# Kernel optimization log

Measured on AMD Instinct MI355X. Metric: run time of the kernel, lower is better.

The kernel has to match this reference:

```python
import jax, jax.numpy as jnp
import numpy as np

HEAD_COUNT = 16


def setup_inputs() -> dict:
    key = jax.random.key(0)
    ks = jax.random.split(key, 9)
    B, T, C = 2, 2048, 1024
    s = 1.0 / np.sqrt(C)
    x = jax.random.normal(ks[0], (B, T, C), dtype=jnp.float32)
    Wq = jax.random.normal(ks[1], (C, C), dtype=jnp.float32) * s
    bq = jnp.zeros((C,), dtype=jnp.float32)
    Wk = jax.random.normal(ks[2], (C, C), dtype=jnp.float32) * s
    bk = jnp.zeros((C,), dtype=jnp.float32)
    Wv = jax.random.normal(ks[3], (C, C), dtype=jnp.float32) * s
    bv = jnp.zeros((C,), dtype=jnp.float32)
    Wp = jax.random.normal(ks[4], (C, C), dtype=jnp.float32) * s
    bp = jnp.zeros((C,), dtype=jnp.float32)
    return {"x": x, "Wq": Wq, "bq": bq, "Wk": Wk, "bk": bk,
            "Wv": Wv, "bv": bv, "Wp": Wp, "bp": bp}


def reference(x, Wq, bq, Wk, bk, Wv, bv, Wp, bp):
    B, T, C = x.shape
    H = HEAD_COUNT
    D = C // H
    # Linear projections (torch Linear: y = x W^T + b) -> [B, H, T, D]
    def proj(W, b):
        y = jnp.einsum('btc,dc->btd', x, W) + b
        return y.reshape(B, T, H, D).transpose(0, 2, 1, 3)
    q = proj(Wq, bq)
    k = proj(Wk, bk)
    v = proj(Wv, bv)
    # Scaled dot-product attention with causal mask
    att = jnp.einsum('bhqd,bhkd->bhqk', q, k) * (1.0 / np.sqrt(D))
    causal = jnp.tril(jnp.ones((T, T), dtype=bool))  # [T, T]
    att = jnp.where(causal[None, None], att, -jnp.inf)
    att = jax.nn.softmax(att, axis=-1)
    # attention dropout p=0.0 (eval equivalent): identity
    y = jnp.einsum('bhqk,bhkd->bhqd', att, v)
    y = y.transpose(0, 2, 1, 3).reshape(B, T, C)
    # output projection + residual dropout p=0.0
    out = jnp.einsum('btc,dc->btd', y, Wp) + bp
    return out
```

## Files before the change

kernel.cpp:

```cpp
#include <hip/hip_runtime.h>
#include <math.h>

#define BATCH 2
#define SEQ   2048
#define CDIM  1024
#define NH    16
#define HD    64

typedef _Float16 half8 __attribute__((ext_vector_type(8)));
typedef _Float16 half4 __attribute__((ext_vector_type(4)));
typedef float    f32x4 __attribute__((ext_vector_type(4)));

#define LDH 72

typedef const __attribute__((address_space(1))) void* gas_ptr;
typedef __attribute__((address_space(3))) void* las_ptr;

__device__ __forceinline__ void gld16(const _Float16* g, _Float16* l) {
    __builtin_amdgcn_global_load_lds((gas_ptr)g, (las_ptr)l, 16, 0, 0);
}

__device__ inline half8 cvt8(float4 a, float4 b) {
    half8 h;
    h[0] = (_Float16)a.x; h[1] = (_Float16)a.y; h[2] = (_Float16)a.z; h[3] = (_Float16)a.w;
    h[4] = (_Float16)b.x; h[5] = (_Float16)b.y; h[6] = (_Float16)b.z; h[7] = (_Float16)b.w;
    return h;
}

__global__ __launch_bounds__(256) void cvt_all(
    const float* __restrict__ x,
    const float* __restrict__ Wq, const float* __restrict__ Wk,
    const float* __restrict__ Wv, const float* __restrict__ Wp,
    _Float16* __restrict__ x16, _Float16* __restrict__ w16,
    _Float16* __restrict__ wp16)
{
    int c = blockIdx.x * 256 + threadIdx.x;
    const float* src;
    _Float16* dst;
    if (c < 524288) {
        src = x + (size_t)c * 8;
        dst = x16 + (size_t)c * 8;
    } else {
        int r = c - 524288;
        int w = r >> 17;
        size_t off = (size_t)(r & 131071) * 8;
        if (w == 0)      { src = Wq + off; dst = w16 + off; }
        else if (w == 1) { src = Wk + off; dst = w16 + (1u << 20) + off; }
        else if (w == 2) { src = Wv + off; dst = w16 + (2u << 20) + off; }
        else             { src = Wp + off; dst = wp16 + off; }
    }
    float4 a = *(const float4*)src;
    float4 b = *(const float4*)(src + 4);
    *(half8*)dst = cvt8(a, b);
}

__global__ __launch_bounds__(256) void qkv_gemm(
    const _Float16* __restrict__ x16, const _Float16* __restrict__ w16,
    const float* __restrict__ bq, const float* __restrict__ bk,
    const float* __restrict__ bv,
    _Float16* __restrict__ q, _Float16* __restrict__ k, _Float16* __restrict__ v)
{
    __shared__ _Float16 Ash[128 * 64];
    __shared__ _Float16 Bsh[128 * 64];

    const int tid  = threadIdx.x;
    const int lane = tid & 63;
    const int wave = tid >> 6;
    const int wm = wave >> 1;
    const int wn = wave & 1;
    const int lg = lane >> 4;
    const int lr = lane & 15;

    const int m0 = blockIdx.x * 128;
    const int nG = blockIdx.y * 128;
    const int w  = nG >> 10;

    const int srow = lane >> 3;
    const int scol = (lane & 7) * 8;

    f32x4 acc[4][4];
#pragma unroll
    for (int m = 0; m < 4; ++m)
#pragma unroll
        for (int n = 0; n < 4; ++n) acc[m][n] = (f32x4)0.0f;

    for (int kt = 0; kt < CDIM; kt += 64) {
        __syncthreads();
#pragma unroll
        for (int i = 0; i < 4; ++i) {
            int chunk = wave * 4 + i;
            int row = chunk * 8 + srow;
            gld16(x16 + (size_t)(m0 + row) * CDIM + kt + scol, Ash + chunk * 512);
            gld16(w16 + (size_t)(nG + row) * CDIM + kt + scol, Bsh + chunk * 512);
        }
        __syncthreads();
#pragma unroll
        for (int kk = 0; kk < 2; ++kk) {
            half8 af[4], bf[4];
#pragma unroll
            for (int m = 0; m < 4; ++m)
                af[m] = *(half8*)&Ash[(wm * 64 + m * 16 + lr) * 64 + kk * 32 + lg * 8];
#pragma unroll
            for (int n = 0; n < 4; ++n)
                bf[n] = *(half8*)&Bsh[(wn * 64 + n * 16 + lr) * 64 + kk * 32 + lg * 8];
#pragma unroll
            for (int m = 0; m < 4; ++m)
#pragma unroll
                for (int n = 0; n < 4; ++n)
                    acc[m][n] = __builtin_amdgcn_mfma_f32_16x16x32_f16(af[m], bf[n], acc[m][n], 0, 0, 0);
        }
    }

    const float* bias = (w == 0) ? bq : (w == 1) ? bk : bv;
    _Float16* dst     = (w == 0) ? q  : (w == 1) ? k  : v;
    const float qs    = (w == 0) ? 0.125f : 1.0f;
    const int n0 = nG & 1023;

#pragma unroll
    for (int n = 0; n < 4; ++n) {
        int col = n0 + wn * 64 + n * 16 + lr;
        float bv_ = bias[col];
        int h = col >> 6, d = col & 63;
#pragma unroll
        for (int m = 0; m < 4; ++m) {
#pragma unroll
            for (int i = 0; i < 4; ++i) {
                int mr = m0 + wm * 64 + m * 16 + lg * 4 + i;
                int bb = mr >> 11;
                int t  = mr & (SEQ - 1);
                dst[((size_t)(bb * NH + h) * SEQ + t) * HD + d] =
                    (_Float16)((acc[m][n][i] + bv_) * qs);
            }
        }
    }
}

__global__ __launch_bounds__(256) void proj_gemm(
    const _Float16* __restrict__ y16, const _Float16* __restrict__ wp16,
    const float* __restrict__ bp, float* __restrict__ out)
{
    __shared__ _Float16 Ash[128 * 64];
    __shared__ _Float16 Bsh[64 * 64];

    const int tid  = threadIdx.x;
    const int lane = tid & 63;
    const int wave = tid >> 6;
    const int wm = wave >> 1;
    const int wn = wave & 1;
    const int lg = lane >> 4;
    const int lr = lane & 15;

    const int m0 = blockIdx.x * 128;
    const int n0 = blockIdx.y * 64;

    const int srow = lane >> 3;
    const int scol = (lane & 7) * 8;

    f32x4 acc[4][2];
#pragma unroll
    for (int m = 0; m < 4; ++m)
#pragma unroll
        for (int n = 0; n < 2; ++n) acc[m][n] = (f32x4)0.0f;

    for (int kt = 0; kt < CDIM; kt += 64) {
        __syncthreads();
#pragma unroll
        for (int i = 0; i < 4; ++i) {
            int chunk = wave * 4 + i;
            int row = chunk * 8 + srow;
            gld16(y16 + (size_t)(m0 + row) * CDIM + kt + scol, Ash + chunk * 512);
        }
#pragma unroll
        for (int i = 0; i < 2; ++i) {
            int chunk = wave * 2 + i;
            int row = chunk * 8 + srow;
            gld16(wp16 + (size_t)(n0 + row) * CDIM + kt + scol, Bsh + chunk * 512);
        }
        __syncthreads();
#pragma unroll
        for (int kk = 0; kk < 2; ++kk) {
            half8 af[4], bf[2];
#pragma unroll
            for (int m = 0; m < 4; ++m)
                af[m] = *(half8*)&Ash[(wm * 64 + m * 16 + lr) * 64 + kk * 32 + lg * 8];
#pragma unroll
            for (int n = 0; n < 2; ++n)
                bf[n] = *(half8*)&Bsh[(wn * 32 + n * 16 + lr) * 64 + kk * 32 + lg * 8];
#pragma unroll
            for (int m = 0; m < 4; ++m)
#pragma unroll
                for (int n = 0; n < 2; ++n)
                    acc[m][n] = __builtin_amdgcn_mfma_f32_16x16x32_f16(af[m], bf[n], acc[m][n], 0, 0, 0);
        }
    }

#pragma unroll
    for (int n = 0; n < 2; ++n) {
        int col = n0 + wn * 32 + n * 16 + lr;
        float bv_ = bp[col];
#pragma unroll
        for (int m = 0; m < 4; ++m) {
#pragma unroll
            for (int i = 0; i < 4; ++i) {
                int mr = m0 + wm * 64 + m * 16 + lg * 4 + i;
                out[(size_t)mr * CDIM + col] = acc[m][n][i] + bv_;
            }
        }
    }
}

__global__ __launch_bounds__(256) void attn_kernel(
    const _Float16* __restrict__ q, const _Float16* __restrict__ k,
    const _Float16* __restrict__ v, _Float16* __restrict__ y)
{
    __shared__ _Float16 Kt[64 * 64];
    __shared__ _Float16 Vt[64 * LDH];
    __shared__ _Float16 Pt[4][32 * LDH];

    const int tid  = threadIdx.x;
    const int lane = tid & 63;
    const int wave = tid >> 6;
    const int lg = lane >> 4;
    const int lr = lane & 15;

    const int qt  = gridDim.x - 1 - blockIdx.x;
    const int bh  = blockIdx.y;
    const int q0  = qt * 128;
    const int q0w = q0 + wave * 32;

    const _Float16* qb = q + (size_t)bh * SEQ * HD;
    const _Float16* kb = k + (size_t)bh * SEQ * HD;
    const _Float16* vb = v + (size_t)bh * SEQ * HD;

    half8 qfr[2][2];
#pragma unroll
    for (int f = 0; f < 2; ++f)
#pragma unroll
        for (int kk = 0; kk < 2; ++kk)
            qfr[f][kk] = *(const half8*)(qb + (size_t)(q0w + f * 16 + lr) * HD + kk * 32 + lg * 8);

    f32x4 ot[4][2];
#pragma unroll
    for (int df = 0; df < 4; ++df)
#pragma unroll
        for (int qf = 0; qf < 2; ++qf) ot[df][qf] = (f32x4)0.0f;
    float m_i[2] = {-INFINITY, -INFINITY};
    float l_i[2] = {0.0f, 0.0f};

    const int vd0  = (tid & 15) * 4;
    const int vkv0 = (tid >> 4) * 4;

    const int ntiles = 2 * qt + 2;
    for (int kt = 0; kt < ntiles; ++kt) {
        const int k0 = kt * 64;
        __syncthreads();
#pragma unroll
        for (int i = 0; i < 2; ++i) {
            int chunk = wave * 2 + i;
            int row = chunk * 8 + (lane >> 3);
            gld16(kb + (size_t)(k0 + row) * HD + (lane & 7) * 8, Kt + chunk * 512);
        }
        {
            half4 r0 = *(const half4*)(vb + (size_t)(k0 + vkv0 + 0) * HD + vd0);
            half4 r1 = *(const half4*)(vb + (size_t)(k0 + vkv0 + 1) * HD + vd0);
            half4 r2 = *(const half4*)(vb + (size_t)(k0 + vkv0 + 2) * HD + vd0);
            half4 r3 = *(const half4*)(vb + (size_t)(k0 + vkv0 + 3) * HD + vd0);
            half4 c;
#pragma unroll
            for (int j = 0; j < 4; ++j) {
                c[0] = r0[j]; c[1] = r1[j]; c[2] = r2[j]; c[3] = r3[j];
                *(half4*)&Vt[(vd0 + j) * LDH + vkv0] = c;
            }
        }
        __syncthreads();

        f32x4 st[4][2];
#pragma unroll
        for (int mf = 0; mf < 4; ++mf)
#pragma unroll
            for (int qf = 0; qf < 2; ++qf) st[mf][qf] = (f32x4)0.0f;
#pragma unroll
        for (int kk = 0; kk < 2; ++kk) {
#pragma unroll
            for (int mf = 0; mf < 4; ++mf) {
                half8 ak = *(half8*)&Kt[(mf * 16 + lr) * 64 + kk * 32 + lg * 8];
#pragma unroll
                for (int qf = 0; qf < 2; ++qf)
                    st[mf][qf] = __builtin_amdgcn_mfma_f32_16x16x32_f16(ak, qfr[qf][kk], st[mf][qf], 0, 0, 0);
            }
        }

        if (k0 + 63 > q0w) {
#pragma unroll
            for (int mf = 0; mf < 4; ++mf)
#pragma unroll
                for (int qf = 0; qf < 2; ++qf)
#pragma unroll
                    for (int i = 0; i < 4; ++i) {
                        int kv = k0 + mf * 16 + lg * 4 + i;
                        int qq = q0w + qf * 16 + lr;
                        if (kv > qq) st[mf][qf][i] = -INFINITY;
                    }
        }

#pragma unroll
        for (int qf = 0; qf < 2; ++qf) {
            float mx = -INFINITY;
#pragma unroll
            for (int mf = 0; mf < 4; ++mf)
#pragma unroll
                for (int i = 0; i < 4; ++i) mx = fmaxf(mx, st[mf][qf][i]);
            mx = fmaxf(mx, __shfl_xor(mx, 16));
            mx = fmaxf(mx, __shfl_xor(mx, 32));
            float nm = fmaxf(m_i[qf], mx);
            float sc = __expf(m_i[qf] - nm);
            m_i[qf] = nm;
            float rs = 0.0f;
#pragma unroll
            for (int mf = 0; mf < 4; ++mf) {
                half4 pk;
#pragma unroll
                for (int i = 0; i < 4; ++i) {
                    float p = __expf(st[mf][qf][i] - nm);
                    rs += p;
                    pk[i] = (_Float16)p;
                }
                *(half4*)&Pt[wave][(qf * 16 + lr) * LDH + mf * 16 + lg * 4] = pk;
            }
            rs += __shfl_xor(rs, 16);
            rs += __shfl_xor(rs, 32);
            l_i[qf] = l_i[qf] * sc + rs;
#pragma unroll
            for (int df = 0; df < 4; ++df)
#pragma unroll
                for (int i = 0; i < 4; ++i) ot[df][qf][i] *= sc;
        }

#pragma unroll
        for (int kk = 0; kk < 2; ++kk) {
            half8 bp_[2];
#pragma unroll
            for (int qf = 0; qf < 2; ++qf)
                bp_[qf] = *(half8*)&Pt[wave][(qf * 16 + lr) * LDH + kk * 32 + lg * 8];
#pragma unroll
            for (int df = 0; df < 4; ++df) {
                half8 av = *(half8*)&Vt[(df * 16 + lr) * LDH + kk * 32 + lg * 8];
#pragma unroll
                for (int qf = 0; qf < 2; ++qf)
                    ot[df][qf] = __builtin_amdgcn_mfma_f32_16x16x32_f16(av, bp_[qf], ot[df][qf], 0, 0, 0);
            }
        }
    }

    const int bb = bh >> 4;
    const int h  = bh & 15;
#pragma unroll
    for (int qf = 0; qf < 2; ++qf) {
        float inv = 1.0f / l_i[qf];
        int t = q0w + qf * 16 + lr;
        _Float16* dst = y + ((size_t)(bb * SEQ + t)) * CDIM + h * HD;
#pragma unroll
        for (int df = 0; df < 4; ++df) {
            half4 o4;
#pragma unroll
            for (int i = 0; i < 4; ++i) o4[i] = (_Float16)(ot[df][qf][i] * inv);
            *(half4*)(dst + df * 16 + lg * 4) = o4;
        }
    }
}

extern "C" void kernel_launch(void* const* d_in, const int* in_sizes, int n_in,
                              void* d_out, int out_size, void* d_ws, size_t ws_size,
                              hipStream_t stream) {
    const float* x  = (const float*)d_in[0];
    const float* Wq = (const float*)d_in[1];
    const float* bq = (const float*)d_in[2];
    const float* Wk = (const float*)d_in[3];
    const float* bk = (const float*)d_in[4];
    const float* Wv = (const float*)d_in[5];
    const float* bv = (const float*)d_in[6];
    const float* Wp = (const float*)d_in[7];
    const float* bp = (const float*)d_in[8];
    float* out = (float*)d_out;

    const size_t S = (size_t)BATCH * SEQ * CDIM;
    _Float16* ws = (_Float16*)d_ws;
    _Float16* x16  = ws;
    _Float16* w16  = x16 + S;
    _Float16* wp16 = w16 + 3 * CDIM * CDIM;
    _Float16* qbuf = wp16 + CDIM * CDIM;
    _Float16* kbuf = qbuf + S;
    _Float16* vbuf = kbuf + S;
    _Float16* ybuf = vbuf + S;

    cvt_all<<<4096, 256, 0, stream>>>(x, Wq, Wk, Wv, Wp, x16, w16, wp16);

    qkv_gemm<<<dim3(4096 / 128, 3072 / 128), 256, 0, stream>>>(
        x16, w16, bq, bk, bv, qbuf, kbuf, vbuf);

    attn_kernel<<<dim3(SEQ / 128, BATCH * NH), 256, 0, stream>>>(
        qbuf, kbuf, vbuf, ybuf);

    proj_gemm<<<dim3(4096 / 128, 1024 / 64), 256, 0, stream>>>(
        ybuf, wp16, bp, out);
}
```

Baseline: 243.5 us.

## Split attention block into eight waves of 16 queries with swizzled K tile

The attention kernel now launches 512 threads per block, so each wave owns 16 query rows instead of 32. This halves per-wave register state and gives more waves to hide latency. Waves whose query rows lie entirely before the current key tile now skip that tile's QK^T, softmax and PV work, which trims causal-mask waste. The K tile in LDS uses an XOR swizzle to reduce bank conflicts, and V staging is split across more threads. In exchange, each K/V tile loaded into LDS is reused by fewer query rows per wave, MFMA operand reuse drops, and the higher thread count may limit occupancy.

Result: faster. 225.6 us (-7.3%).

```diff
diff --git a/kernel.cpp b/kernel.cpp
--- a/kernel.cpp
+++ b/kernel.cpp
@@ -9,6 +9,7 @@
 
 typedef _Float16 half8 __attribute__((ext_vector_type(8)));
 typedef _Float16 half4 __attribute__((ext_vector_type(4)));
+typedef _Float16 half2v __attribute__((ext_vector_type(2)));
 typedef float    f32x4 __attribute__((ext_vector_type(4)));
 
 #define LDH 72
@@ -209,13 +210,13 @@
     }
 }
 
-__global__ __launch_bounds__(256) void attn_kernel(
+__global__ __launch_bounds__(512) void attn_kernel(
     const _Float16* __restrict__ q, const _Float16* __restrict__ k,
     const _Float16* __restrict__ v, _Float16* __restrict__ y)
 {
     __shared__ _Float16 Kt[64 * 64];
     __shared__ _Float16 Vt[64 * LDH];
-    __shared__ _Float16 Pt[4][32 * LDH];
+    __shared__ _Float16 Pt[8][16 * LDH];
 
     const int tid  = threadIdx.x;
     const int lane = tid & 63;
@@ -226,146 +227,121 @@
     const int qt  = gridDim.x - 1 - blockIdx.x;
     const int bh  = blockIdx.y;
     const int q0  = qt * 128;
-    const int q0w = q0 + wave * 32;
+    const int q0w = q0 + wave * 16;
 
     const _Float16* qb = q + (size_t)bh * SEQ * HD;
     const _Float16* kb = k + (size_t)bh * SEQ * HD;
     const _Float16* vb = v + (size_t)bh * SEQ * HD;
 
-    half8 qfr[2][2];
-#pragma unroll
-    for (int f = 0; f < 2; ++f)
-#pragma unroll
-        for (int kk = 0; kk < 2; ++kk)
-            qfr[f][kk] = *(const half8*)(qb + (size_t)(q0w + f * 16 + lr) * HD + kk * 32 + lg * 8);
-
-    f32x4 ot[4][2];
-#pragma unroll
-    for (int df = 0; df < 4; ++df)
-#pragma unroll
-        for (int qf = 0; qf < 2; ++qf) ot[df][qf] = (f32x4)0.0f;
-    float m_i[2] = {-INFINITY, -INFINITY};
-    float l_i[2] = {0.0f, 0.0f};
-
+    half8 qfr[2];
+#pragma unroll
+    for (int kk = 0; kk < 2; ++kk)
+        qfr[kk] = *(const half8*)(qb + (size_t)(q0w + lr) * HD + kk * 32 + lg * 8);
+
+    f32x4 ot[4];
+#pragma unroll
+    for (int df = 0; df < 4; ++df) ot[df] = (f32x4)0.0f;
+    float m_i = -INFINITY;
+    float l_i = 0.0f;
+
+    const int krow  = wave * 8 + (lane >> 3);
+    const int kunit = (lane & 7) ^ (lane >> 3);
     const int vd0  = (tid & 15) * 4;
-    const int vkv0 = (tid >> 4) * 4;
+    const int vkv0 = (tid >> 4) * 2;
 
     const int ntiles = 2 * qt + 2;
     for (int kt = 0; kt < ntiles; ++kt) {
         const int k0 = kt * 64;
         __syncthreads();
-#pragma unroll
-        for (int i = 0; i < 2; ++i) {
-            int chunk = wave * 2 + i;
-            int row = chunk * 8 + (lane >> 3);
-            gld16(kb + (size_t)(k0 + row) * HD + (lane & 7) * 8, Kt + chunk * 512);
-        }
+        gld16(kb + (size_t)(k0 + krow) * HD + kunit * 8, Kt + wave * 512);
         {
             half4 r0 = *(const half4*)(vb + (size_t)(k0 + vkv0 + 0) * HD + vd0);
             half4 r1 = *(const half4*)(vb + (size_t)(k0 + vkv0 + 1) * HD + vd0);
-            half4 r2 = *(const half4*)(vb + (size_t)(k0 + vkv0 + 2) * HD + vd0);
-            half4 r3 = *(const half4*)(vb + (size_t)(k0 + vkv0 + 3) * HD + vd0);
-            half4 c;
 #pragma unroll
             for (int j = 0; j < 4; ++j) {
-                c[0] = r0[j]; c[1] = r1[j]; c[2] = r2[j]; c[3] = r3[j];
-                *(half4*)&Vt[(vd0 + j) * LDH + vkv0] = c;
-            }
-        }
-        __syncthreads();
-
-        f32x4 st[4][2];
-#pragma unroll
-        for (int mf = 0; mf < 4; ++mf)
-#pragma unroll
-            for (int qf = 0; qf < 2; ++qf) st[mf][qf] = (f32x4)0.0f;
-#pragma unroll
-        for (int kk = 0; kk < 2; ++kk) {
-#pragma unroll
-            for (int mf = 0; mf < 4; ++mf) {
-                half8 ak = *(half8*)&Kt[(mf * 16 + lr) * 64 + kk * 32 + lg * 8];
-#pragma unroll
-                for (int qf = 0; qf < 2; ++qf)
-                    st[mf][qf] = __builtin_amdgcn_mfma_f32_16x16x32_f16(ak, qfr[qf][kk], st[mf][qf], 0, 0, 0);
-            }
-        }
-
-        if (k0 + 63 > q0w) {
-#pragma unroll
-            for (int mf = 0; mf < 4; ++mf)
-#pragma unroll
-                for (int qf = 0; qf < 2; ++qf)
+                half2v c2; c2[0] = r0[j]; c2[1] = r1[j];
+                *(half2v*)&Vt[(vd0 + j) * LDH + vkv0] = c2;
+            }
+        }
+        __syncthreads();
+
+        if (k0 <= q0w + 15) {
+            f32x4 st[4];
+#pragma unroll
+            for (int mf = 0; mf < 4; ++mf) st[mf] = (f32x4)0.0f;
+#pragma unroll
+            for (int kk = 0; kk < 2; ++kk) {
+#pragma unroll
+                for (int mf = 0; mf < 4; ++mf) {
+                    half8 ak = *(half8*)&Kt[(mf * 16 + lr) * 64 +
+                                            (((kk * 4 + lg) ^ (lr & 7)) * 8)];
+                    st[mf] = __builtin_amdgcn_mfma_f32_16x16x32_f16(ak, qfr[kk], st[mf], 0, 0, 0);
+                }
+            }
+
+            if (k0 + 63 > q0w) {
+#pragma unroll
+                for (int mf = 0; mf < 4; ++mf)
 #pragma unroll
                     for (int i = 0; i < 4; ++i) {
                         int kv = k0 + mf * 16 + lg * 4 + i;
-                        int qq = q0w + qf * 16 + lr;
-                        if (kv > qq) st[mf][qf][i] = -INFINITY;
+                        if (kv > q0w + lr) st[mf][i] = -INFINITY;
                     }
-        }
-
-#pragma unroll
-        for (int qf = 0; qf < 2; ++qf) {
+            }
+
             float mx = -INFINITY;
 #pragma unroll
             for (int mf = 0; mf < 4; ++mf)
 #pragma unroll
-                for (int i = 0; i < 4; ++i) mx = fmaxf(mx, st[mf][qf][i]);
+                for (int i = 0; i < 4; ++i) mx = fmaxf(mx, st[mf][i]);
             mx = fmaxf(mx, __shfl_xor(mx, 16));
             mx = fmaxf(mx, __shfl_xor(mx, 32));
-            float nm = fmaxf(m_i[qf], mx);
-            float sc = __expf(m_i[qf] - nm);
-            m_i[qf] = nm;
+            float nm = fmaxf(m_i, mx);
+            float sc = __expf(m_i - nm);
+            m_i = nm;
             float rs = 0.0f;
 #pragma unroll
             for (int mf = 0; mf < 4; ++mf) {
                 half4 pk;
 #pragma unroll
                 for (int i = 0; i < 4; ++i) {
-                    float p = __expf(st[mf][qf][i] - nm);
+                    float p = __expf(st[mf][i] - nm);
                     rs += p;
                     pk[i] = (_Float16)p;
                 }
-                *(half4*)&Pt[wave][(qf * 16 + lr) * LDH + mf * 16 + lg * 4] = pk;
+                *(half4*)&Pt[wave][lr * LDH + mf * 16 + lg * 4] = pk;
             }
             rs += __shfl_xor(rs, 16);
             rs += __shfl_xor(rs, 32);
-            l_i[qf] = l_i[qf] * sc + rs;
+            l_i = l_i * sc + rs;
 #pragma unroll
             for (int df = 0; df < 4; ++df)
 #pragma unroll
-                for (int i = 0; i < 4; ++i) ot[df][qf][i] *= sc;
-        }
-
-#pragma unroll
-        for (int kk = 0; kk < 2; ++kk) {
-            half8 bp_[2];
-#pragma unroll
-            for (int qf = 0; qf < 2; ++qf)
-                bp_[qf] = *(half8*)&Pt[wave][(qf * 16 + lr) * LDH + kk * 32 + lg * 8];
-#pragma unroll
-            for (int df = 0; df < 4; ++df) {
-                half8 av = *(half8*)&Vt[(df * 16 + lr) * LDH + kk * 32 + lg * 8];
-#pragma unroll
-                for (int qf = 0; qf < 2; ++qf)
-                    ot[df][qf] = __builtin_amdgcn_mfma_f32_16x16x32_f16(av, bp_[qf], ot[df][qf], 0, 0, 0);
+                for (int i = 0; i < 4; ++i) ot[df][i] *= sc;
+
+#pragma unroll
+            for (int kk = 0; kk < 2; ++kk) {
+                half8 bp_ = *(half8*)&Pt[wave][lr * LDH + kk * 32 + lg * 8];
+#pragma unroll
+                for (int df = 0; df < 4; ++df) {
+                    half8 av = *(half8*)&Vt[(df * 16 + lr) * LDH + kk * 32 + lg * 8];
+                    ot[df] = __builtin_amdgcn_mfma_f32_16x16x32_f16(av, bp_, ot[df], 0, 0, 0);
+                }
             }
         }
     }
 
     const int bb = bh >> 4;
     const int h  = bh & 15;
-#pragma unroll
-    for (int qf = 0; qf < 2; ++qf) {
-        float inv = 1.0f / l_i[qf];
-        int t = q0w + qf * 16 + lr;
-        _Float16* dst = y + ((size_t)(bb * SEQ + t)) * CDIM + h * HD;
-#pragma unroll
-        for (int df = 0; df < 4; ++df) {
-            half4 o4;
-#pragma unroll
-            for (int i = 0; i < 4; ++i) o4[i] = (_Float16)(ot[df][qf][i] * inv);
-            *(half4*)(dst + df * 16 + lg * 4) = o4;
-        }
+    float inv = 1.0f / l_i;
+    int t = q0w + lr;
+    _Float16* dst = y + ((size_t)(bb * SEQ + t)) * CDIM + h * HD;
+#pragma unroll
+    for (int df = 0; df < 4; ++df) {
+        half4 o4;
+#pragma unroll
+        for (int i = 0; i < 4; ++i) o4[i] = (_Float16)(ot[df][i] * inv);
+        *(half4*)(dst + df * 16 + lg * 4) = o4;
     }
 }
 
@@ -398,7 +374,7 @@
     qkv_gemm<<<dim3(4096 / 128, 3072 / 128), 256, 0, stream>>>(
         x16, w16, bq, bk, bv, qbuf, kbuf, vbuf);
 
-    attn_kernel<<<dim3(SEQ / 128, BATCH * NH), 256, 0, stream>>>(
+    attn_kernel<<<dim3(SEQ / 128, BATCH * NH), 512, 0, stream>>>(
         qbuf, kbuf, vbuf, ybuf);
 
     proj_gemm<<<dim3(4096 / 128, 1024 / 64), 256, 0, stream>>>(
```
